# Optimization experiments

Measured on AMD Instinct MI355X. Metric: run time of the kernel, lower is better.

The kernel has to match this reference:

```python
import jax, jax.numpy as jnp
import numpy as np

EPS = 1e-5

def _conv(x, w, b, stride, pad):
    y = jax.lax.conv_general_dilated(
        x, w, window_strides=(stride, stride),
        padding=[(pad, pad), (pad, pad)],
        dimension_numbers=('NCHW', 'OIHW', 'NCHW'))
    return y + b.reshape(1, -1, 1, 1)

def _bn(x, gamma, beta):
    # training-mode batch norm: per-channel batch statistics over (N, H, W)
    mean = jnp.mean(x, axis=(0, 2, 3), keepdims=True)
    var = jnp.var(x, axis=(0, 2, 3), keepdims=True)
    xn = (x - mean) * jax.lax.rsqrt(var + EPS)
    return gamma.reshape(1, -1, 1, 1) * xn + beta.reshape(1, -1, 1, 1)

def setup_inputs() -> dict:
    key = jax.random.key(0)
    ks = jax.random.split(key, 8)
    N, Cin, H, W = 64, 1024, 14, 14
    P = 256                      # planes (bottleneck width)
    Cout = P * 4                 # expansion = 4 -> 1024
    def kaiming(k, shape):
        fan_in = shape[1] * shape[2] * shape[3]
        return jax.random.normal(k, shape, jnp.float32) * np.float32(np.sqrt(2.0 / fan_in))
    return {
        'x':  jax.random.normal(ks[0], (N, Cin, H, W), jnp.float32),
        'w1': kaiming(ks[1], (P, Cin, 1, 1)),  'b1': jnp.zeros((P,), jnp.float32),
        'g1': jnp.ones((P,), jnp.float32),     'be1': jnp.zeros((P,), jnp.float32),
        'w2': kaiming(ks[2], (P, P, 3, 3)),    'b2': jnp.zeros((P,), jnp.float32),
        'g2': jnp.ones((P,), jnp.float32),     'be2': jnp.zeros((P,), jnp.float32),
        'w3': kaiming(ks[3], (Cout, P, 1, 1)), 'b3': jnp.zeros((Cout,), jnp.float32),
        'g3': jnp.ones((Cout,), jnp.float32),  'be3': jnp.zeros((Cout,), jnp.float32),
        'residual_scale': jnp.zeros((1,), jnp.float32),
    }

def reference(x, w1, b1, g1, be1, w2, b2, g2, be2, w3, b3, g3, be3, residual_scale):
    out = jax.nn.relu(_bn(_conv(x, w1, b1, 1, 0), g1, be1))   # 1x1 reduce
    out = jax.nn.relu(_bn(_conv(out, w2, b2, 1, 1), g2, be2)) # 3x3
    out = _bn(_conv(out, w3, b3, 1, 0), g3, be3)              # 1x1 expand
    out = jax.nn.softplus(residual_scale)[0] * out            # scaled residual branch
    out = x + out                                             # identity shortcut (stride=1, Cin==Cout)
    return jax.nn.relu(out)
```

## Files before the change

### kernel.cpp

```cpp
#include <hip/hip_runtime.h>
#include <hip/hip_bf16.h>
#include <cstdint>

#define NB   64
#define CIN  1024
#define HWSP 196
#define MTOT 12544
#define PL   256
#define COUT 1024

using f32x4 = __attribute__((ext_vector_type(4))) float;
using s16x8 = __attribute__((ext_vector_type(8))) short;

static __device__ __forceinline__ short f2bf(float f) {
  union { __hip_bfloat16 h; short s; } u;
  u.h = __float2bfloat16(f);
  return u.s;
}
static __device__ __forceinline__ float bf2f(short s) {
  union { float f; unsigned u; } x;
  x.u = ((unsigned)(unsigned short)s) << 16;
  return x.f;
}

static __device__ __forceinline__ void gload16(const void* g, void* l) {
  __builtin_amdgcn_global_load_lds((const __attribute__((address_space(1))) void*)g,
                                   (__attribute__((address_space(3))) void*)l, 16, 0, 0);
}

__global__ __launch_bounds__(256) void k_prep(const float* __restrict__ x,
                                              const float* __restrict__ w1,
                                              const float* __restrict__ w2,
                                              const float* __restrict__ w3,
                                              short* __restrict__ xb,
                                              short* __restrict__ w1b,
                                              short* __restrict__ w2b,
                                              short* __restrict__ w3b,
                                              float* __restrict__ statszero) {
  const int bid = blockIdx.x;
  if (bid < 2048) {
    __shared__ float tile[32][197];
    const int n = bid >> 5;
    const int c0 = (bid & 31) * 32;
    for (int idx = threadIdx.x; idx < 32 * 196; idx += 256) {
      int cl = idx / 196, hw = idx % 196;
      tile[cl][hw] = x[((size_t)(n * CIN + c0 + cl)) * HWSP + hw];
    }
    __syncthreads();
    for (int idx = threadIdx.x; idx < 196 * 32; idx += 256) {
      int hw = idx >> 5, cl = idx & 31;
      xb[((size_t)(n * HWSP + hw)) * CIN + c0 + cl] = f2bf(tile[cl][hw]);
    }
  } else if (bid < 6400) {
    int i = (bid - 2048) * 256 + threadIdx.x;
    if (i < 262144) w1b[i] = f2bf(w1[i]);
    int j = i - 262144;
    if (j >= 0 && j < 589824) {
      int co = j / 2304, rem = j % 2304;
      int d = rem >> 8, ci = rem & 255;
      w2b[j] = f2bf(w2[((size_t)(co * 256 + ci)) * 9 + d]);
    }
    int k = i - 851968;
    if (k >= 0 && k < 262144) w3b[k] = f2bf(w3[k]);
  } else {
    for (int k = threadIdx.x; k < 3136; k += 256) statszero[k] = 0.f;
  }
}

static __device__ __forceinline__ int swz(int row, int k16, int bk) {
  return row * (bk * 2) + (((unsigned)(k16 ^ (row & 7))) << 4);
}

template <int MODE, int K, int BK>
__global__ __launch_bounds__(256) void gemm_kernel(const short* __restrict__ A,
                                                   const short* __restrict__ Bw,
                                                   const float* __restrict__ bias,
                                                   short* __restrict__ Yb,
                                                   float* __restrict__ st,
                                                   int Nc,
                                                   const short* __restrict__ zerobuf) {
  constexpr int NKT = K / BK;
  constexpr int KCH = BK / 8;
  constexpr int QN = BK / 16;
  constexpr int TBYTES = 128 * BK * 2;
  __shared__ __align__(16) char lds[2][2 * TBYTES];

  const int m0 = blockIdx.x * 128;
  const int n0 = blockIdx.y * 128;
  const int t = threadIdx.x;
  const int lane = t & 63, wid = t >> 6;
  const int wm = wid >> 1, wn = wid & 1;
  const int g = lane >> 4, r = lane & 15;

  const short* aSrc[QN];
  int aN[QN], aH[QN], aW[QN], aCi[QN];
  const short* bSrc[QN];
#pragma unroll
  for (int q = 0; q < QN; ++q) {
    int chunk = t + q * 256;
    int row = chunk / KCH;
    int k16s = (chunk % KCH) ^ (row & 7);
    if (MODE == 0) {
      aSrc[q] = A + (size_t)(m0 + row) * K + k16s * 8;
    } else {
      int m = m0 + row;
      int n_ = m / 196;
      int hw = m - n_ * 196;
      aN[q] = n_;
      aH[q] = hw / 14;
      aW[q] = hw - aH[q] * 14;
      aCi[q] = k16s * 8;
    }
    bSrc[q] = Bw + (size_t)(n0 + row) * K + k16s * 8;
  }

  auto stage = [&](int buf, int kt) {
    const int k0 = kt * BK;
    char* dA = &lds[buf][0];
    char* dB = &lds[buf][TBYTES];
#pragma unroll
    for (int q = 0; q < QN; ++q) {
      const short* s;
      if (MODE == 0) {
        s = aSrc[q] + k0;
      } else {
        int d = k0 >> 8;
        int dh = d / 3, dw = d - dh * 3;
        int hh = aH[q] + dh - 1, ww = aW[q] + dw - 1;
        s = ((unsigned)hh < 14u && (unsigned)ww < 14u)
                ? A + ((size_t)(aN[q] * 196 + hh * 14 + ww)) * 256 + (k0 & 255) + aCi[q]
                : zerobuf;
      }
      gload16(s, dA + (t + q * 256) * 16);
    }
#pragma unroll
    for (int q = 0; q < QN; ++q)
      gload16(bSrc[q] + k0, dB + (t + q * 256) * 16);
  };

  f32x4 acc[4][4] = {};
  auto compute = [&](int buf) {
    char* baseA = &lds[buf][0];
    char* baseB = &lds[buf][TBYTES];
#pragma unroll
    for (int ks = 0; ks < BK / 32; ++ks) {
      s16x8 af[4], bfr[4];
#pragma unroll
      for (int i = 0; i < 4; ++i)
        af[i] = *(const s16x8*)(baseA + swz(wm * 64 + i * 16 + r, ks * 4 + g, BK));
#pragma unroll
      for (int j = 0; j < 4; ++j)
        bfr[j] = *(const s16x8*)(baseB + swz(wn * 64 + j * 16 + r, ks * 4 + g, BK));
#pragma unroll
      for (int i = 0; i < 4; ++i)
#pragma unroll
        for (int j = 0; j < 4; ++j)
          acc[i][j] = __builtin_amdgcn_mfma_f32_16x16x32_bf16(af[i], bfr[j], acc[i][j], 0, 0, 0);
    }
  };

  stage(0, 0);
  int cur = 0;
#pragma unroll 1
  for (int kt = 0; kt < NKT - 1; ++kt) {
    stage(cur ^ 1, kt + 1);
    if constexpr (BK == 64)
      asm volatile("s_waitcnt vmcnt(8)" ::: "memory");
    else
      asm volatile("s_waitcnt vmcnt(16)" ::: "memory");
    __builtin_amdgcn_s_barrier();
    compute(cur);
    asm volatile("" ::: "memory");
    __builtin_amdgcn_s_barrier();
    cur ^= 1;
  }
  asm volatile("s_waitcnt vmcnt(0)" ::: "memory");
  __builtin_amdgcn_s_barrier();
  compute(cur);

#pragma unroll
  for (int j = 0; j < 4; ++j) {
    int col = n0 + wn * 64 + j * 16 + r;
    float bv = bias[col];
    float ps = 0.f, pq = 0.f;
#pragma unroll
    for (int i = 0; i < 4; ++i) {
      int row_base = m0 + wm * 64 + i * 16 + g * 4;
#pragma unroll
      for (int rr = 0; rr < 4; ++rr) {
        float v = acc[i][j][rr] + bv;
        ps += v;
        pq += v * v;
        Yb[(size_t)(row_base + rr) * Nc + col] = f2bf(v);
      }
    }
    ps += __shfl_xor(ps, 16);
    ps += __shfl_xor(ps, 32);
    pq += __shfl_xor(pq, 16);
    pq += __shfl_xor(pq, 32);
    if (lane < 16) {
      atomicAdd(&st[col], ps);
      atomicAdd(&st[Nc + col], pq);
    }
  }
}

__global__ __launch_bounds__(256) void k_apply(short* __restrict__ Yb,
                                               const float* __restrict__ st,
                                               const float* __restrict__ gamma,
                                               const float* __restrict__ beta) {
  __shared__ float lsc[256], lsh[256];
  const int t = threadIdx.x;
  {
    const float inv = 1.0f / 12544.0f;
    float mean = st[t] * inv;
    float var = st[256 + t] * inv - mean * mean;
    float s = gamma[t] * rsqrtf(var + 1e-5f);
    lsc[t] = s;
    lsh[t] = beta[t] - mean * s;
  }
  __syncthreads();
  size_t i8 = ((size_t)blockIdx.x * 256 + t) * 8;
  s16x8 v = *(const s16x8*)(Yb + i8);
  int c0 = (int)(i8 & 255);
#pragma unroll
  for (int e = 0; e < 8; ++e) {
    float f = bf2f(v[e]);
    v[e] = f2bf(fmaxf(lsc[c0 + e] * f + lsh[c0 + e], 0.f));
  }
  *(s16x8*)(Yb + i8) = v;
}

__global__ __launch_bounds__(256) void k_final(const float* __restrict__ x,
                                               const short* __restrict__ y3b,
                                               const float* __restrict__ st,
                                               const float* __restrict__ gamma,
                                               const float* __restrict__ beta,
                                               const float* __restrict__ rs,
                                               float* __restrict__ out) {
  __shared__ short ytile[64][198];
  __shared__ float lsc[64], lsh[64];
  const int n = blockIdx.x;
  const int co0 = blockIdx.y * 64;
  const int t = threadIdx.x;
  if (t < 64) {
    const float inv = 1.0f / 12544.0f;
    int c = co0 + t;
    float mean = st[c] * inv;
    float var = st[1024 + c] * inv - mean * mean;
    float s = gamma[c] * rsqrtf(var + 1e-5f);
    lsc[t] = s;
    lsh[t] = beta[c] - mean * s;
  }
#pragma unroll
  for (int iter = 0; iter < 49; ++iter) {
    int idx = iter * 256 + t;
    int hw = idx >> 6, c = idx & 63;
    ytile[c][hw] = y3b[((size_t)(n * 196 + hw)) * 1024 + co0 + c];
  }
  __syncthreads();
  float z = rs[0];
  float s = fmaxf(z, 0.f) + log1pf(expf(-fabsf(z)));
#pragma unroll
  for (int iter = 0; iter < 49; ++iter) {
    int idx = iter * 256 + t;
    int co = idx / 196, hw = idx - co * 196;
    size_t xi = ((size_t)(n * 1024 + co0 + co)) * 196 + hw;
    float v = bf2f(ytile[co][hw]);
    float o = x[xi] + s * (lsc[co] * v + lsh[co]);
    out[xi] = fmaxf(o, 0.f);
  }
}

extern "C" void kernel_launch(void* const* d_in, const int* in_sizes, int n_in,
                              void* d_out, int out_size, void* d_ws, size_t ws_size,
                              hipStream_t stream) {
  const float* x   = (const float*)d_in[0];
  const float* w1  = (const float*)d_in[1];
  const float* b1  = (const float*)d_in[2];
  const float* g1  = (const float*)d_in[3];
  const float* be1 = (const float*)d_in[4];
  const float* w2  = (const float*)d_in[5];
  const float* b2  = (const float*)d_in[6];
  const float* g2  = (const float*)d_in[7];
  const float* be2 = (const float*)d_in[8];
  const float* w3  = (const float*)d_in[9];
  const float* b3  = (const float*)d_in[10];
  const float* g3  = (const float*)d_in[11];
  const float* be3 = (const float*)d_in[12];
  const float* rs  = (const float*)d_in[13];
  float* out = (float*)d_out;
  char* ws = (char*)d_ws;

  size_t off = 0;
  auto alloc = [&](size_t bytes) {
    size_t o = off;
    off += (bytes + 255) & ~(size_t)255;
    return o;
  };
  short* xb  = (short*)(ws + alloc((size_t)MTOT * CIN * 2));
  short* w1b = (short*)(ws + alloc((size_t)262144 * 2));
  short* w2b = (short*)(ws + alloc((size_t)589824 * 2));
  short* w3b = (short*)(ws + alloc((size_t)262144 * 2));
  short* y1b = (short*)(ws + alloc((size_t)MTOT * PL * 2));
  short* y2b = (short*)(ws + alloc((size_t)MTOT * PL * 2));
  short* y3b = (short*)(ws + alloc((size_t)MTOT * COUT * 2));
  float* stats = (float*)(ws + alloc(12288 + 256));
  float* stat1 = stats, *stat2 = stats + 512, *stat3 = stats + 1024;
  short* zerobuf = (short*)(stats + 3072);

  k_prep<<<6401, 256, 0, stream>>>(x, w1, w2, w3, xb, w1b, w2b, w3b, stats);

  gemm_kernel<0, 1024, 128><<<dim3(98, 2), 256, 0, stream>>>(xb, w1b, b1, y1b, stat1, 256, zerobuf);
  k_apply<<<1568, 256, 0, stream>>>(y1b, stat1, g1, be1);

  gemm_kernel<1, 2304, 128><<<dim3(98, 2), 256, 0, stream>>>(y1b, w2b, b2, y2b, stat2, 256, zerobuf);
  k_apply<<<1568, 256, 0, stream>>>(y2b, stat2, g2, be2);

  gemm_kernel<0, 256, 64><<<dim3(98, 8), 256, 0, stream>>>(y2b, w3b, b3, y3b, stat3, 1024, zerobuf);

  k_final<<<dim3(64, 16), 256, 0, stream>>>(x, y3b, stat3, g3, be3, rs, out);
}
```

Before: 124.1 us.

## Stage conv2 input halo once in LDS and reuse across all nine taps

Adds a dedicated 3x3 conv kernel that loads the block's 128 output rows plus a 15-row halo of y1 activations (all 256 channels) into LDS once. The 9 taps then index into that tile with shifted row offsets instead of re-gathering im2col chunks from global memory for every k-tile. Only the weight tile is double-buffered, using a smaller K-step of 64. This cuts repeated global A-loads and per-tap address and bounds computation. In exchange it uses about 80 KB of LDS per block, which lowers occupancy, and the halo rows come from the flat image index range with a zero row standing in for out-of-bounds taps.

```diff
diff --git a/kernel.cpp b/kernel.cpp
--- a/kernel.cpp
+++ b/kernel.cpp
@@ -71,14 +71,13 @@
   return row * (bk * 2) + (((unsigned)(k16 ^ (row & 7))) << 4);
 }
 
-template <int MODE, int K, int BK>
+template <int K, int BK>
 __global__ __launch_bounds__(256) void gemm_kernel(const short* __restrict__ A,
                                                    const short* __restrict__ Bw,
                                                    const float* __restrict__ bias,
                                                    short* __restrict__ Yb,
                                                    float* __restrict__ st,
-                                                   int Nc,
-                                                   const short* __restrict__ zerobuf) {
+                                                   int Nc) {
   constexpr int NKT = K / BK;
   constexpr int KCH = BK / 8;
   constexpr int QN = BK / 16;
@@ -93,24 +92,13 @@
   const int g = lane >> 4, r = lane & 15;
 
   const short* aSrc[QN];
-  int aN[QN], aH[QN], aW[QN], aCi[QN];
   const short* bSrc[QN];
 #pragma unroll
   for (int q = 0; q < QN; ++q) {
     int chunk = t + q * 256;
     int row = chunk / KCH;
     int k16s = (chunk % KCH) ^ (row & 7);
-    if (MODE == 0) {
-      aSrc[q] = A + (size_t)(m0 + row) * K + k16s * 8;
-    } else {
-      int m = m0 + row;
-      int n_ = m / 196;
-      int hw = m - n_ * 196;
-      aN[q] = n_;
-      aH[q] = hw / 14;
-      aW[q] = hw - aH[q] * 14;
-      aCi[q] = k16s * 8;
-    }
+    aSrc[q] = A + (size_t)(m0 + row) * K + k16s * 8;
     bSrc[q] = Bw + (size_t)(n0 + row) * K + k16s * 8;
   }
 
@@ -119,20 +107,8 @@
     char* dA = &lds[buf][0];
     char* dB = &lds[buf][TBYTES];
 #pragma unroll
-    for (int q = 0; q < QN; ++q) {
-      const short* s;
-      if (MODE == 0) {
-        s = aSrc[q] + k0;
-      } else {
-        int d = k0 >> 8;
-        int dh = d / 3, dw = d - dh * 3;
-        int hh = aH[q] + dh - 1, ww = aW[q] + dw - 1;
-        s = ((unsigned)hh < 14u && (unsigned)ww < 14u)
-                ? A + ((size_t)(aN[q] * 196 + hh * 14 + ww)) * 256 + (k0 & 255) + aCi[q]
-                : zerobuf;
-      }
-      gload16(s, dA + (t + q * 256) * 16);
-    }
+    for (int q = 0; q < QN; ++q)
+      gload16(aSrc[q] + k0, dA + (t + q * 256) * 16);
 #pragma unroll
     for (int q = 0; q < QN; ++q)
       gload16(bSrc[q] + k0, dB + (t + q * 256) * 16);
@@ -201,6 +177,132 @@
     if (lane < 16) {
       atomicAdd(&st[col], ps);
       atomicAdd(&st[Nc + col], pq);
+    }
+  }
+}
+
+__global__ __launch_bounds__(256) void k_conv2(const short* __restrict__ y1b,
+                                               const short* __restrict__ w2b,
+                                               const float* __restrict__ bias,
+                                               short* __restrict__ Yb,
+                                               float* __restrict__ st,
+                                               const short* __restrict__ zerobuf) {
+  __shared__ __align__(16) char ldsA[159 * 512];
+  __shared__ __align__(16) char ldsB[2][16384];
+
+  const int m0 = blockIdx.x * 128;
+  const int n0 = blockIdx.y * 128;
+  const int t = threadIdx.x;
+  const int lane = t & 63, wid = t >> 6;
+  const int wm = wid >> 1, wn = wid & 1;
+  const int g = lane >> 4, r = lane & 15;
+
+  const int lo = (m0 >= 15) ? m0 - 15 : 0;
+  const int hi = (m0 + 143 < MTOT) ? m0 + 143 : MTOT;
+  const int nch = (hi - lo) * 32;
+
+#pragma unroll
+  for (int q = 0; q < 20; ++q) {
+    int chunk = t + q * 256;
+    if (chunk < nch) {
+      int row = chunk >> 5, k16d = chunk & 31;
+      int k16s = k16d ^ (row & 7);
+      gload16(y1b + (size_t)(lo + row) * 256 + k16s * 8, ldsA + chunk * 16);
+    }
+  }
+  if (t < 32) gload16(zerobuf, ldsA + (158 * 32 + t) * 16);
+
+  const short* bSrc[4];
+#pragma unroll
+  for (int q = 0; q < 4; ++q) {
+    int chunk = t + q * 256;
+    int row = chunk >> 3;
+    int k16s = (chunk & 7) ^ (row & 7);
+    bSrc[q] = w2b + (size_t)(n0 + row) * 2304 + k16s * 8;
+  }
+  auto stageB = [&](int buf, int kt) {
+#pragma unroll
+    for (int q = 0; q < 4; ++q)
+      gload16(bSrc[q] + kt * 64, ldsB[buf] + (t + q * 256) * 16);
+  };
+
+  int mrel[4], hc[4], wc[4];
+#pragma unroll
+  for (int i = 0; i < 4; ++i) {
+    int m = m0 + wm * 64 + i * 16 + r;
+    mrel[i] = m - lo;
+    int hw = m % 196;
+    hc[i] = hw / 14;
+    wc[i] = hw - hc[i] * 14;
+  }
+
+  stageB(0, 0);
+  asm volatile("s_waitcnt vmcnt(0)" ::: "memory");
+  __builtin_amdgcn_s_barrier();
+
+  f32x4 acc[4][4] = {};
+  int cur = 0;
+#pragma unroll 1
+  for (int kt = 0; kt < 36; ++kt) {
+    int d = kt >> 2, cb = kt & 3;
+    int dh = d / 3, dw = d - dh * 3;
+    int off = (dh - 1) * 14 + (dw - 1);
+    int rowi[4];
+#pragma unroll
+    for (int i = 0; i < 4; ++i) {
+      int hh = hc[i] + dh - 1, ww = wc[i] + dw - 1;
+      bool v = ((unsigned)hh < 14u) && ((unsigned)ww < 14u);
+      rowi[i] = v ? (mrel[i] + off) : 158;
+    }
+    if (kt < 35) stageB(cur ^ 1, kt + 1);
+    asm volatile("s_waitcnt vmcnt(4)" ::: "memory");
+    __builtin_amdgcn_s_barrier();
+#pragma unroll
+    for (int ks = 0; ks < 2; ++ks) {
+      s16x8 af[4], bfr[4];
+#pragma unroll
+      for (int i = 0; i < 4; ++i) {
+        int k16 = cb * 8 + ks * 4 + g;
+        af[i] = *(const s16x8*)(ldsA + rowi[i] * 512 +
+                                (((unsigned)(k16 ^ (rowi[i] & 7))) << 4));
+      }
+#pragma unroll
+      for (int j = 0; j < 4; ++j)
+        bfr[j] = *(const s16x8*)(ldsB[cur] + swz(wn * 64 + j * 16 + r, ks * 4 + g, 64));
+#pragma unroll
+      for (int i = 0; i < 4; ++i)
+#pragma unroll
+        for (int j = 0; j < 4; ++j)
+          acc[i][j] = __builtin_amdgcn_mfma_f32_16x16x32_bf16(af[i], bfr[j], acc[i][j], 0, 0, 0);
+    }
+    asm volatile("" ::: "memory");
+    __builtin_amdgcn_s_barrier();
+    cur ^= 1;
+  }
+
+#pragma unroll
+  for (int j = 0; j < 4; ++j) {
+    int col = n0 + wn * 64 + j * 16 + r;
+    float bv = bias[col];
+    float ps = 0.f, pq = 0.f;
+#pragma unroll
+    for (int i = 0; i < 4; ++i) {
+      int row_base = m0 + wm * 64 + i * 16 + g * 4;
+#pragma unroll
+      for (int rr = 0; rr < 4; ++rr) {
+        float v = acc[i][j][rr] + bv;
+        ps += v;
+        pq += v * v;
+        Yb[(size_t)(row_base + rr) * 256 + col] = f2bf(v);
+      }
+    }
+    ps += __shfl_xor(ps, 16);
+    ps += __shfl_xor(ps, 32);
+    pq += __shfl_xor(pq, 16);
+    pq += __shfl_xor(pq, 32);
+    if (lane < 16) {
+      atomicAdd(&st[col], ps);
+      atomicAdd(&st[256 + col], pq);
     }
   }
 }
@@ -311,13 +413,13 @@
 
   k_prep<<<6401, 256, 0, stream>>>(x, w1, w2, w3, xb, w1b, w2b, w3b, stats);
 
-  gemm_kernel<0, 1024, 128><<<dim3(98, 2), 256, 0, stream>>>(xb, w1b, b1, y1b, stat1, 256, zerobuf);
+  gemm_kernel<1024, 128><<<dim3(98, 2), 256, 0, stream>>>(xb, w1b, b1, y1b, stat1, 256);
   k_apply<<<1568, 256, 0, stream>>>(y1b, stat1, g1, be1);
 
-  gemm_kernel<1, 2304, 128><<<dim3(98, 2), 256, 0, stream>>>(y1b, w2b, b2, y2b, stat2, 256, zerobuf);
+  k_conv2<<<dim3(98, 2), 256, 0, stream>>>(y1b, w2b, b2, y2b, stat2, zerobuf);
   k_apply<<<1568, 256, 0, stream>>>(y2b, stat2, g2, be2);
 
-  gemm_kernel<0, 256, 64><<<dim3(98, 8), 256, 0, stream>>>(y2b, w3b, b3, y3b, stat3, 1024, zerobuf);
+  gemm_kernel<256, 64><<<dim3(98, 8), 256, 0, stream>>>(y2b, w3b, b3, y3b, stat3, 1024);
 
   k_final<<<dim3(64, 16), 256, 0, stream>>>(x, y3b, stat3, g3, be3, rs, out);
 }
```

After: 127.2 us. +2.4%, slower.
